# Performance work log

Hardware: AMD Instinct MI355X
Metric: run time of the kernel (lower is better)

Reference implementation:

```python
import jax, jax.numpy as jnp
import numpy as np

# Config (BERT-base with T5-style shared relative attention bias)
B, S, D, H, F, V, L = 16, 512, 768, 12, 3072, 30522, 12
DH = D // H
MAXREL = 128  # bias table has 2*MAXREL+1 = 257 buckets
EPS = 1e-12


def layer_norm(x, w, b):
    mu = jnp.mean(x, axis=-1, keepdims=True)
    var = jnp.mean(jnp.square(x - mu), axis=-1, keepdims=True)
    return (x - mu) * jax.lax.rsqrt(var + EPS) * w + b


def setup_inputs() -> dict:
    key = jax.random.key(0)
    ks = jax.random.split(key, 16)
    s = 0.02
    inp = {
        "input_ids": jax.random.randint(ks[0], (B, S), 0, V),
        "attention_mask": jnp.ones((B, S), jnp.float32),
        "word_emb": jax.random.normal(ks[1], (V, D), jnp.float32) * s,
        "pos_emb": jax.random.normal(ks[2], (S, D), jnp.float32) * s,
        "emb_ln_w": jnp.ones((D,), jnp.float32),
        "emb_ln_b": jnp.zeros((D,), jnp.float32),
        "rel_bias_table": jax.random.normal(ks[3], (2 * MAXREL + 1, H), jnp.float32) * s,
        "Wq": jax.random.normal(ks[4], (L, D, D), jnp.float32) * s,
        "bq": jnp.zeros((L, D), jnp.float32),
        "Wk": jax.random.normal(ks[5], (L, D, D), jnp.float32) * s,
        "bk": jnp.zeros((L, D), jnp.float32),
        "Wv": jax.random.normal(ks[6], (L, D, D), jnp.float32) * s,
        "bv": jnp.zeros((L, D), jnp.float32),
        "Wo": jax.random.normal(ks[7], (L, D, D), jnp.float32) * s,
        "bo": jnp.zeros((L, D), jnp.float32),
        "attn_ln_w": jnp.ones((L, D), jnp.float32),
        "attn_ln_b": jnp.zeros((L, D), jnp.float32),
        "Wi": jax.random.normal(ks[8], (L, F, D), jnp.float32) * s,
        "bi": jnp.zeros((L, F), jnp.float32),
        "Wd": jax.random.normal(ks[9], (L, D, F), jnp.float32) * s,
        "bd": jnp.zeros((L, D), jnp.float32),
        "out_ln_w": jnp.ones((L, D), jnp.float32),
        "out_ln_b": jnp.zeros((L, D), jnp.float32),
    }
    return inp


def _encoder(input_ids, attention_mask, word_emb, pos_emb, emb_ln_w, emb_ln_b,
             rel_bias_table, Wq, bq, Wk, bk, Wv, bv, Wo, bo, attn_ln_w, attn_ln_b,
             Wi, bi, Wd, bd, out_ln_w, out_ln_b):
    b, s = input_ids.shape
    # Embeddings: word + learned absolute position, then LayerNorm
    h = word_emb[input_ids] + pos_emb[:s][None, :, :]
    h = layer_norm(h, emb_ln_w, emb_ln_b)

    # Shared relative position bias: [H, S, S]
    pos = jnp.arange(s)
    rel = jnp.clip(pos[None, :] - pos[:, None], -MAXREL, MAXREL) + MAXREL
    rel_bias = jnp.transpose(rel_bias_table[rel], (2, 0, 1))[None]  # [1,H,S,S]

    # Additive attention mask: [B,1,1,S]
    add_mask = (1.0 - attention_mask)[:, None, None, :] * -10000.0
    scale = 1.0 / np.sqrt(DH)

    def step(h, p):
        wq, bq_, wk, bk_, wv, bv_, wo, bo_, lw1, lb1, wi, bi_, wd, bd_, lw2, lb2 = p
        q = (h @ wq.T + bq_).reshape(b, s, H, DH)
        k = (h @ wk.T + bk_).reshape(b, s, H, DH)
        v = (h @ wv.T + bv_).reshape(b, s, H, DH)
        scores = jnp.einsum('bqhd,bkhd->bhqk', q, k) * scale + rel_bias + add_mask
        attn = jax.nn.softmax(scores, axis=-1)
        ctx = jnp.einsum('bhqk,bkhd->bqhd', attn, v).reshape(b, s, D)
        h1 = layer_norm(h + (ctx @ wo.T + bo_), lw1, lb1)
        inter = jax.nn.gelu(h1 @ wi.T + bi_, approximate=False)
        h2 = layer_norm(h1 + (inter @ wd.T + bd_), lw2, lb2)
        return h2, None

    params = (Wq, bq, Wk, bk, Wv, bv, Wo, bo, attn_ln_w, attn_ln_b,
              Wi, bi, Wd, bd, out_ln_w, out_ln_b)
    h, _ = jax.lax.scan(step, h, params)
    return h


def reference(input_ids, attention_mask, word_emb, pos_emb, emb_ln_w, emb_ln_b,
              rel_bias_table, Wq, bq, Wk, bk, Wv, bv, Wo, bo, attn_ln_w, attn_ln_b,
              Wi, bi, Wd, bd, out_ln_w, out_ln_b):
    return _encoder(input_ids, attention_mask, word_emb, pos_emb, emb_ln_w, emb_ln_b,
                    rel_bias_table, Wq, bq, Wk, bk, Wv, bv, Wo, bo, attn_ln_w, attn_ln_b,
                    Wi, bi, Wd, bd, out_ln_w, out_ln_b)
```

## Files before the change

kernel.cpp:

```cpp
#include <hip/hip_runtime.h>
#include <cstdint>
#include <cstddef>

#define BB 16
#define SS 512
#define DD 768
#define HH 12
#define FF 3072
#define LL 12
#define DHD 64
#define MM (BB*SS)

typedef __attribute__((ext_vector_type(8))) short bf16x8;
typedef __attribute__((ext_vector_type(4))) float f32x4;

__device__ __forceinline__ ushort f2bf(float f) {
  union { float f; uint32_t u; } x; x.f = f;
  uint32_t r = x.u + 0x7FFFu + ((x.u >> 16) & 1u);
  return (ushort)(r >> 16);
}
__device__ __forceinline__ float bf2f(ushort u) {
  union { uint32_t u; float f; } x; x.u = (uint32_t)u << 16;
  return x.f;
}

__device__ __forceinline__ void glds16(const ushort* g, ushort* l) {
  __builtin_amdgcn_global_load_lds((__attribute__((address_space(1))) void*)g,
                                   (__attribute__((address_space(3))) void*)l,
                                   16, 0, 0);
}

__device__ __forceinline__ float gelu_t(float v) {
  const float v2 = v * v;
  const float u = v * (-1.5957691216f - 0.0713548163f * v2);
  return v / (1.f + __expf(u));
}

__global__ __launch_bounds__(256)
void convw6(const float* __restrict__ s0, const float* __restrict__ s1,
            const float* __restrict__ s2, const float* __restrict__ s3,
            const float* __restrict__ s4, const float* __restrict__ s5,
            ushort* __restrict__ dA, ushort* __restrict__ dB, int perD, int perF)
{
  const int y = blockIdx.y;
  const int per = (y < 4) ? perD : perF;
  const int i = (blockIdx.x * 256 + threadIdx.x) * 4;
  if (i >= per) return;
  const float* s = y == 0 ? s0 : y == 1 ? s1 : y == 2 ? s2 : y == 3 ? s3 : y == 4 ? s4 : s5;
  ushort* dst = (y < 4) ? (dA + (size_t)y * perD) : (dB + (size_t)(y - 4) * perF);
  const float4 v = *(const float4*)(s + i);
  ushort4 o;
  o.x = f2bf(v.x); o.y = f2bf(v.y); o.z = f2bf(v.z); o.w = f2bf(v.w);
  *(ushort4*)(dst + i) = o;
}

__global__ __launch_bounds__(256)
void embed_ln_kernel(const int* __restrict__ ids, const float* __restrict__ wemb,
                     const float* __restrict__ pemb, const float* __restrict__ g,
                     const float* __restrict__ bt, float* __restrict__ hf,
                     ushort* __restrict__ hb)
{
  const int row = blockIdx.x;
  const int s = row & (SS - 1);
  const int id = ids[row];
  const float* wp = wemb + (size_t)id * DD;
  const float* pp = pemb + (size_t)s * DD;
  const int tid = threadIdx.x;
  float v[3]; float sum = 0.f, sq = 0.f;
#pragma unroll
  for (int j = 0; j < 3; ++j) {
    int e = tid + j * 256;
    v[j] = wp[e] + pp[e];
    sum += v[j]; sq += v[j] * v[j];
  }
  __shared__ float red[2][4];
#pragma unroll
  for (int off = 32; off >= 1; off >>= 1) { sum += __shfl_xor(sum, off); sq += __shfl_xor(sq, off); }
  const int lane = tid & 63, wid = tid >> 6;
  if (lane == 0) { red[0][wid] = sum; red[1][wid] = sq; }
  __syncthreads();
  sum = red[0][0] + red[0][1] + red[0][2] + red[0][3];
  sq  = red[1][0] + red[1][1] + red[1][2] + red[1][3];
  const float mean = sum * (1.f / DD);
  const float var  = sq  * (1.f / DD) - mean * mean;
  const float rstd = rsqrtf(var + 1e-12f);
  const size_t base = (size_t)row * DD;
#pragma unroll
  for (int j = 0; j < 3; ++j) {
    int e = tid + j * 256;
    float o = (v[j] - mean) * rstd * g[e] + bt[e];
    hf[base + e] = o;
    hb[base + e] = f2bf(o);
  }
}

__global__ __launch_bounds__(256)
void add_ln2_kernel(const float* __restrict__ res, const ushort* __restrict__ p0,
                    const ushort* __restrict__ p1, const float* __restrict__ g,
                    const float* __restrict__ bt, float* __restrict__ hf,
                    ushort* __restrict__ hb)
{
  const int row = blockIdx.x;
  const int tid = threadIdx.x;
  const size_t base = (size_t)row * DD;
  float v[3]; float sum = 0.f, sq = 0.f;
#pragma unroll
  for (int j = 0; j < 3; ++j) {
    int e = tid + j * 256;
    v[j] = res[base + e] + bf2f(p0[base + e]) + bf2f(p1[base + e]);
    sum += v[j]; sq += v[j] * v[j];
  }
  __shared__ float red[2][4];
#pragma unroll
  for (int off = 32; off >= 1; off >>= 1) { sum += __shfl_xor(sum, off); sq += __shfl_xor(sq, off); }
  const int lane = tid & 63, wid = tid >> 6;
  if (lane == 0) { red[0][wid] = sum; red[1][wid] = sq; }
  __syncthreads();
  sum = red[0][0] + red[0][1] + red[0][2] + red[0][3];
  sq  = red[1][0] + red[1][1] + red[1][2] + red[1][3];
  const float mean = sum * (1.f / DD);
  const float var  = sq  * (1.f / DD) - mean * mean;
  const float rstd = rsqrtf(var + 1e-12f);
#pragma unroll
  for (int j = 0; j < 3; ++j) {
    int e = tid + j * 256;
    float o = (v[j] - mean) * rstd * g[e] + bt[e];
    hf[base + e] = o;
    hb[base + e] = f2bf(o);
  }
}

template<int EPI, bool TRV>
__global__ __launch_bounds__(256, 4)
void gemm_ker(const ushort* __restrict__ A,
              const ushort* __restrict__ B0, const ushort* __restrict__ B1,
              const ushort* __restrict__ B2,
              const float* __restrict__ bias0, const float* __restrict__ bias1,
              const float* __restrict__ bias2,
              void* __restrict__ C0, void* __restrict__ C1, void* __restrict__ C2,
              int Kdim, int nblk)
{
  __shared__ ushort As[2][128 * 32];
  __shared__ ushort Bs[2][128 * 32];

  int id = blockIdx.y * gridDim.x + blockIdx.x;
  const int chunk = (gridDim.x * gridDim.y) >> 3;
  id = (id & 7) * chunk + (id >> 3);
  const int bm = id & 63;
  const int bnAll = id >> 6;
  const int sub = bnAll / nblk;
  const int bn = bnAll - sub * nblk;

  const ushort* Bw  = sub == 0 ? B0 : (sub == 1 ? B1 : B2);
  const float* bias = sub == 0 ? bias0 : (sub == 1 ? bias1 : bias2);
  const int Ndim = nblk * 128;

  const int tid = threadIdx.x;
  const int l = tid & 63, w = tid >> 6;
  const int wm = w >> 1, wn = w & 1;
  const int fr = l & 15, fg = l >> 4;

  const int srow_in = l >> 2;
  const int gks = ((l & 3) ^ ((l >> 3) & 3)) * 8;
  const ushort* Agl0 = A  + (size_t)(bm * 128 + w * 16 + srow_in) * Kdim + gks;
  const ushort* Agl1 = Agl0 + (size_t)64 * Kdim;
  const ushort* Bgl0 = Bw + (size_t)(bn * 128 + w * 16 + srow_in) * Kdim + gks;
  const ushort* Bgl1 = Bgl0 + (size_t)64 * Kdim;

  auto stage = [&](int b, int kt) {
    const int ko = kt * 32;
    ushort* al = &As[b][w * 64 * 8];
    ushort* bl = &Bs[b][w * 64 * 8];
    glds16(Agl0 + ko, al);
    glds16(Agl1 + ko, al + 256 * 8);
    glds16(Bgl0 + ko, bl);
    glds16(Bgl1 + ko, bl + 256 * 8);
  };

  const int se = (fg ^ ((fr >> 1) & 3)) * 8;

  f32x4 acc[4][4];
#pragma unroll
  for (int i = 0; i < 4; ++i)
#pragma unroll
    for (int j = 0; j < 4; ++j) acc[i][j] = f32x4{0.f, 0.f, 0.f, 0.f};

  stage(0, 0);
  __syncthreads();

  const int nk = Kdim >> 5;
  int cur = 0;
  for (int kt = 0; kt < nk; ++kt) {
    if (kt + 1 < nk) stage(cur ^ 1, kt + 1);

    bf16x8 af[4], bfv[4];
#pragma unroll
    for (int i = 0; i < 4; ++i)
      af[i]  = *(const bf16x8*)&As[cur][(wm * 64 + i * 16 + fr) * 32 + se];
#pragma unroll
    for (int j = 0; j < 4; ++j)
      bfv[j] = *(const bf16x8*)&Bs[cur][(wn * 64 + j * 16 + fr) * 32 + se];

    __builtin_amdgcn_s_setprio(1);
#pragma unroll
    for (int i = 0; i < 4; ++i)
#pragma unroll
      for (int j = 0; j < 4; ++j)
        acc[i][j] = __builtin_amdgcn_mfma_f32_16x16x32_bf16(bfv[j], af[i], acc[i][j], 0, 0, 0);
    __builtin_amdgcn_s_setprio(0);

    __syncthreads();
    cur ^= 1;
  }

#pragma unroll
  for (int i = 0; i < 4; ++i) {
    const int row_g = bm * 128 + wm * 64 + i * 16 + fr;
#pragma unroll
    for (int j = 0; j < 4; ++j) {
      const int col = bn * 128 + wn * 64 + j * 16 + fg * 4;
      const float4 bv4 = *(const float4*)&bias[col];
      const float v0 = acc[i][j][0] + bv4.x;
      const float v1 = acc[i][j][1] + bv4.y;
      const float v2 = acc[i][j][2] + bv4.z;
      const float v3 = acc[i][j][3] + bv4.w;
      if (TRV && sub == 2) {
        const int b_ = row_g >> 9, s_ = row_g & 511;
        const int h_ = col >> 6, d0 = col & 63;
        ushort* vp = (ushort*)C2 + (((size_t)(b_ * HH + h_) * DHD + d0) * SS + s_);
        vp[0] = f2bf(v0); vp[SS] = f2bf(v1); vp[2 * SS] = f2bf(v2); vp[3 * SS] = f2bf(v3);
      } else if (EPI == 2) {
        ushort4 o4;
        o4.x = f2bf(gelu_t(v0)); o4.y = f2bf(gelu_t(v1));
        o4.z = f2bf(gelu_t(v2)); o4.w = f2bf(gelu_t(v3));
        *(ushort4*)&((ushort*)C0)[(size_t)row_g * Ndim + col] = o4;
      } else {
        void* Cout = sub == 0 ? C0 : (sub == 1 ? C1 : C2);
        ushort4 o4;
        o4.x = f2bf(v0); o4.y = f2bf(v1); o4.z = f2bf(v2); o4.w = f2bf(v3);
        *(ushort4*)&((ushort*)Cout)[(size_t)row_g * Ndim + col] = o4;
      }
    }
  }
}

__global__ __launch_bounds__(256, 4)
void gemm_sk(const ushort* __restrict__ A, const ushort* __restrict__ Bw,
             const float* __restrict__ bias, ushort* __restrict__ P0,
             ushort* __restrict__ P1, int Kdim)
{
  __shared__ ushort As[2][128 * 32];
  __shared__ ushort Bs[2][128 * 32];

  int id = blockIdx.y * gridDim.x + blockIdx.x;
  const int chunk = (gridDim.x * gridDim.y) >> 3;
  id = (id & 7) * chunk + (id >> 3);
  const int bm = id & 63;
  const int rest = id >> 6;
  const int bn = rest >> 1;
  const int sk = rest & 1;

  const int Kh = Kdim >> 1;

  const int tid = threadIdx.x;
  const int l = tid & 63, w = tid >> 6;
  const int wm = w >> 1, wn = w & 1;
  const int fr = l & 15, fg = l >> 4;

  const int srow_in = l >> 2;
  const int gks = ((l & 3) ^ ((l >> 3) & 3)) * 8;
  const ushort* Agl0 = A  + (size_t)(bm * 128 + w * 16 + srow_in) * Kdim + sk * Kh + gks;
  const ushort* Agl1 = Agl0 + (size_t)64 * Kdim;
  const ushort* Bgl0 = Bw + (size_t)(bn * 128 + w * 16 + srow_in) * Kdim + sk * Kh + gks;
  const ushort* Bgl1 = Bgl0 + (size_t)64 * Kdim;

  auto stage = [&](int b, int kt) {
    const int ko = kt * 32;
    ushort* al = &As[b][w * 64 * 8];
    ushort* bl = &Bs[b][w * 64 * 8];
    glds16(Agl0 + ko, al);
    glds16(Agl1 + ko, al + 256 * 8);
    glds16(Bgl0 + ko, bl);
    glds16(Bgl1 + ko, bl + 256 * 8);
  };

  const int se = (fg ^ ((fr >> 1) & 3)) * 8;

  f32x4 acc[4][4];
#pragma unroll
  for (int i = 0; i < 4; ++i)
#pragma unroll
    for (int j = 0; j < 4; ++j) acc[i][j] = f32x4{0.f, 0.f, 0.f, 0.f};

  stage(0, 0);
  __syncthreads();

  const int nk = Kh >> 5;
  int cur = 0;
  for (int kt = 0; kt < nk; ++kt) {
    if (kt + 1 < nk) stage(cur ^ 1, kt + 1);

    bf16x8 af[4], bfv[4];
#pragma unroll
    for (int i = 0; i < 4; ++i)
      af[i]  = *(const bf16x8*)&As[cur][(wm * 64 + i * 16 + fr) * 32 + se];
#pragma unroll
    for (int j = 0; j < 4; ++j)
      bfv[j] = *(const bf16x8*)&Bs[cur][(wn * 64 + j * 16 + fr) * 32 + se];

    __builtin_amdgcn_s_setprio(1);
#pragma unroll
    for (int i = 0; i < 4; ++i)
#pragma unroll
      for (int j = 0; j < 4; ++j)
        acc[i][j] = __builtin_amdgcn_mfma_f32_16x16x32_bf16(bfv[j], af[i], acc[i][j], 0, 0, 0);
    __builtin_amdgcn_s_setprio(0);

    __syncthreads();
    cur ^= 1;
  }

  ushort* P = sk ? P1 : P0;
  const float bs = sk ? 0.f : 1.f;
#pragma unroll
  for (int i = 0; i < 4; ++i) {
    const int row_g = bm * 128 + wm * 64 + i * 16 + fr;
#pragma unroll
    for (int j = 0; j < 4; ++j) {
      const int col = bn * 128 + wn * 64 + j * 16 + fg * 4;
      const float4 bv4 = *(const float4*)&bias[col];
      ushort4 o4;
      o4.x = f2bf(acc[i][j][0] + bv4.x * bs);
      o4.y = f2bf(acc[i][j][1] + bv4.y * bs);
      o4.z = f2bf(acc[i][j][2] + bv4.z * bs);
      o4.w = f2bf(acc[i][j][3] + bv4.w * bs);
      *(ushort4*)&P[(size_t)row_g * DD + col] = o4;
    }
  }
}

__global__ __launch_bounds__(512, 2)
void attn_kernel(const ushort* __restrict__ qb, const ushort* __restrict__ kb,
                 const ushort* __restrict__ vt, const float* __restrict__ relt,
                 const float* __restrict__ amask, ushort* __restrict__ ctxb)
{
  __shared__ ushort Kt[128][72];
  __shared__ ushort Vt[64][136];
  __shared__ ushort Pl[128][136];
  __shared__ float am_lds[512];
  __shared__ float rel_lds[1024];

  const int tid = threadIdx.x, lane = tid & 63, w = tid >> 6;

  int lin = blockIdx.y * gridDim.x + blockIdx.x;
  lin = (lin & 7) * 96 + (lin >> 3);
  const int qt = lin & 3;
  const int bh = lin >> 2;
  const int b = bh / HH, h = bh - b * HH;
  const int fr = lane & 15, fg = lane >> 4;

  am_lds[tid] = (1.0f - amask[b * SS + tid]) * -10000.0f;
  {
    int d0 = tid - 512;
    d0 = max(-128, d0);
    rel_lds[tid] = relt[(d0 + 128) * HH + h];
    int d1 = tid;
    d1 = min(128, d1);
    rel_lds[tid + 512] = relt[(d1 + 128) * HH + h];
  }

  bf16x8 qf[2];
  {
    const int qrow = qt * 128 + w * 16 + fr;
    const ushort* p = qb + ((size_t)(b * SS + qrow) * DD) + h * DHD + fg * 8;
    qf[0] = *(const bf16x8*)p;
    qf[1] = *(const bf16x8*)(p + 32);
  }

  f32x4 o[4];
  float mrow[4], lrow[4];
#pragma unroll
  for (int r = 0; r < 4; ++r) { mrow[r] = -1e30f; lrow[r] = 0.f; }
#pragma unroll
  for (int d = 0; d < 4; ++d) o[d] = f32x4{0.f, 0.f, 0.f, 0.f};

  const int skr = tid >> 2;
  const int shd = (tid & 3) * 16;
  const int vrow = tid >> 3;
  const int vcg  = (tid & 7) * 16;
  const ushort* vgl = vt + ((size_t)bh * DHD + vrow) * SS + vcg;

  const int qg0 = qt * 128 + w * 16;

  for (int kt = 0; kt < 4; ++kt) {
    const size_t gbase = ((size_t)(b * SS + kt * 128 + skr) * DD) + h * DHD + shd;
    int4 kr0 = *(const int4*)(kb + gbase);
    int4 kr1 = *(const int4*)(kb + gbase + 8);
    const ushort* vp = vgl + kt * 128;
    int4 vr0 = *(const int4*)(vp);
    int4 vr1 = *(const int4*)(vp + 8);

    __syncthreads();
    *(int4*)&Kt[skr][shd]     = kr0;
    *(int4*)&Kt[skr][shd + 8] = kr1;
    *(int4*)&Vt[vrow][vcg]     = vr0;
    *(int4*)&Vt[vrow][vcg + 8] = vr1;
    __syncthreads();

    float sv[8][4];
    __builtin_amdgcn_s_setprio(1);
#pragma unroll
    for (int kc = 0; kc < 8; ++kc) {
      f32x4 s = f32x4{0.f, 0.f, 0.f, 0.f};
      bf16x8 kf0 = *(const bf16x8*)&Kt[kc * 16 + fr][fg * 8];
      bf16x8 kf1 = *(const bf16x8*)&Kt[kc * 16 + fr][32 + fg * 8];
      s = __builtin_amdgcn_mfma_f32_16x16x32_bf16(qf[0], kf0, s, 0, 0, 0);
      s = __builtin_amdgcn_mfma_f32_16x16x32_bf16(qf[1], kf1, s, 0, 0, 0);
      const int col = kt * 128 + kc * 16 + fr;
      const float am = am_lds[col];
      const int ridx = col - qg0 - fg * 4 + 512;
#pragma unroll
      for (int r = 0; r < 4; ++r)
        sv[kc][r] = s[r] * 0.125f + rel_lds[ridx - r] + am;
    }
    __builtin_amdgcn_s_setprio(0);

    float ef[4];
#pragma unroll
    for (int r = 0; r < 4; ++r) {
      float tmax = sv[0][r];
#pragma unroll
      for (int kc = 1; kc < 8; ++kc) tmax = fmaxf(tmax, sv[kc][r]);
#pragma unroll
      for (int off = 1; off < 16; off <<= 1) tmax = fmaxf(tmax, __shfl_xor(tmax, off));
      const float mnew = fmaxf(mrow[r], tmax);
      ef[r] = __expf(mrow[r] - mnew);
      float psum = 0.f;
      const int prow = w * 16 + fg * 4 + r;
#pragma unroll
      for (int kc = 0; kc < 8; ++kc) {
        float p = __expf(sv[kc][r] - mnew);
        psum += p;
        Pl[prow][kc * 16 + fr] = f2bf(p);
      }
#pragma unroll
      for (int off = 1; off < 16; off <<= 1) psum += __shfl_xor(psum, off);
      lrow[r] = lrow[r] * ef[r] + psum;
      mrow[r] = mnew;
    }
#pragma unroll
    for (int dc = 0; dc < 4; ++dc)
#pragma unroll
      for (int r = 0; r < 4; ++r) o[dc][r] *= ef[r];
    __syncthreads();

    __builtin_amdgcn_s_setprio(1);
#pragma unroll
    for (int dc = 0; dc < 4; ++dc)
#pragma unroll
      for (int ks = 0; ks < 4; ++ks) {
        bf16x8 pf = *(const bf16x8*)&Pl[w * 16 + fr][ks * 32 + fg * 8];
        bf16x8 vf = *(const bf16x8*)&Vt[dc * 16 + fr][ks * 32 + fg * 8];
        o[dc] = __builtin_amdgcn_mfma_f32_16x16x32_bf16(pf, vf, o[dc], 0, 0, 0);
      }
    __builtin_amdgcn_s_setprio(0);
  }

#pragma unroll
  for (int dc = 0; dc < 4; ++dc)
#pragma unroll
    for (int r = 0; r < 4; ++r) {
      const int qg = qt * 128 + w * 16 + fg * 4 + r;
      const float v = o[dc][r] / lrow[r];
      ctxb[((size_t)(b * SS + qg) * DD) + h * DHD + dc * 16 + fr] = f2bf(v);
    }
}

extern "C" void kernel_launch(void* const* d_in, const int* in_sizes, int n_in,
                              void* d_out, int out_size, void* d_ws, size_t ws_size,
                              hipStream_t stream) {
  const int*   ids   = (const int*)d_in[0];
  const float* amask = (const float*)d_in[1];
  const float* wemb  = (const float*)d_in[2];
  const float* pemb  = (const float*)d_in[3];
  const float* eln_w = (const float*)d_in[4];
  const float* eln_b = (const float*)d_in[5];
  const float* relt  = (const float*)d_in[6];
  const float* Wq    = (const float*)d_in[7];
  const float* bq    = (const float*)d_in[8];
  const float* Wk    = (const float*)d_in[9];
  const float* bk    = (const float*)d_in[10];
  const float* Wv    = (const float*)d_in[11];
  const float* bv    = (const float*)d_in[12];
  const float* Wo    = (const float*)d_in[13];
  const float* bo    = (const float*)d_in[14];
  const float* aln_w = (const float*)d_in[15];
  const float* aln_b = (const float*)d_in[16];
  const float* Wi    = (const float*)d_in[17];
  const float* bi    = (const float*)d_in[18];
  const float* Wd    = (const float*)d_in[19];
  const float* bd    = (const float*)d_in[20];
  const float* oln_w = (const float*)d_in[21];
  const float* oln_b = (const float*)d_in[22];

  size_t off = 0;
  auto carve = [&](size_t bytes) -> void* {
    void* r = (char*)d_ws + off;
    off += (bytes + 255) & ~(size_t)255;
    return r;
  };
  float*  hf     = (float*) carve((size_t)MM * DD * 4);
  ushort* hb     = (ushort*)carve((size_t)MM * DD * 2);
  ushort* qbuf   = (ushort*)carve((size_t)MM * DD * 2);
  ushort* kbuf   = (ushort*)carve((size_t)MM * DD * 2);
  ushort* vbuf   = (ushort*)carve((size_t)MM * DD * 2);
  ushort* ctxb   = (ushort*)carve((size_t)MM * DD * 2);
  ushort* gout   = (ushort*)carve((size_t)MM * DD * 2);
  ushort* gout2  = (ushort*)carve((size_t)MM * DD * 2);
  ushort* interb = (ushort*)carve((size_t)MM * FF * 2);
  const int PD = DD * DD;
  const int PF = FF * DD;
  ushort* wBded  = (ushort*)carve((size_t)2 * PF * 2);

  ushort* wA = interb;

  embed_ln_kernel<<<MM, 256, 0, stream>>>(ids, wemb, pemb, eln_w, eln_b, hf, hb);

  const dim3 gQKV(MM / 128, 3 * (DD / 128));
  const dim3 gSK(MM / 128, 2 * (DD / 128));
  const dim3 gF(MM / 128, FF / 128);
  const dim3 gA(SS / 128, BB * HH);
  const dim3 gC(PF / 1024, 6);

  for (int l = 0; l < LL; ++l) {
    const size_t wo  = (size_t)l * PD;
    const size_t wio = (size_t)l * PF;

    convw6<<<gC, 256, 0, stream>>>(Wq + wo, Wk + wo, Wv + wo, Wo + wo,
                                   Wi + wio, Wd + wio, wA, wBded, PD, PF);

    gemm_ker<0, true><<<gQKV, 256, 0, stream>>>(hb, wA, wA + PD, wA + 2 * PD,
                                                bq + l * DD, bk + l * DD, bv + l * DD,
                                                qbuf, kbuf, vbuf, DD, DD / 128);

    attn_kernel<<<gA, 512, 0, stream>>>(qbuf, kbuf, vbuf, relt, amask, ctxb);

    gemm_sk<<<gSK, 256, 0, stream>>>(ctxb, wA + 3 * PD, bo + l * DD, gout, gout2, DD);
    add_ln2_kernel<<<MM, 256, 0, stream>>>(hf, gout, gout2,
                                           aln_w + l * DD, aln_b + l * DD, hf, hb);

    gemm_ker<2, false><<<gF, 256, 0, stream>>>(hb, wBded, wBded, wBded,
                                               bi + l * FF, bi + l * FF, bi + l * FF,
                                               interb, interb, interb, DD, FF / 128);
    gemm_sk<<<gSK, 256, 0, stream>>>(interb, wBded + PF, bd + l * DD, gout, gout2, FF);

    float* outp = (l == LL - 1) ? (float*)d_out : hf;
    add_ln2_kernel<<<MM, 256, 0, stream>>>(hf, gout, gout2,
                                           oln_w + l * DD, oln_b + l * DD, outp, hb);
  }
}
```

Baseline: 3.355 ms.

## Enlarge GEMM M-tile to 256 rows with 128x64 per-wave tiles

The main GEMM kernel's block tile grows from 128x128 to 256x128. Each wave now computes a 128x64 sub-tile with 32 accumulators instead of 16, and the QKV and FFN-up grids are halved along M. This raises the MFMA-to-LDS-load ratio and reuses each B tile across more rows, cutting shared-memory and global traffic per flop. The cost is more registers and LDS per block, so launch bounds drop to 2 blocks per CU, and fewer blocks may leave occupancy or tail balance worse.

```diff
diff --git a/kernel.cpp b/kernel.cpp
--- a/kernel.cpp
+++ b/kernel.cpp
@@ -131,7 +131,7 @@
 }
 
 template<int EPI, bool TRV>
-__global__ __launch_bounds__(256, 4)
+__global__ __launch_bounds__(256, 2)
 void gemm_ker(const ushort* __restrict__ A,
               const ushort* __restrict__ B0, const ushort* __restrict__ B1,
               const ushort* __restrict__ B2,
@@ -140,14 +140,14 @@
               void* __restrict__ C0, void* __restrict__ C1, void* __restrict__ C2,
               int Kdim, int nblk)
 {
-  __shared__ ushort As[2][128 * 32];
+  __shared__ ushort As[2][256 * 32];
   __shared__ ushort Bs[2][128 * 32];
 
   int id = blockIdx.y * gridDim.x + blockIdx.x;
   const int chunk = (gridDim.x * gridDim.y) >> 3;
   id = (id & 7) * chunk + (id >> 3);
-  const int bm = id & 63;
-  const int bnAll = id >> 6;
+  const int bm = id & 31;
+  const int bnAll = id >> 5;
   const int sub = bnAll / nblk;
   const int bn = bnAll - sub * nblk;
 
@@ -157,31 +157,32 @@
 
   const int tid = threadIdx.x;
   const int l = tid & 63, w = tid >> 6;
-  const int wm = w >> 1, wn = w & 1;
+  const int wr = w & 1, wc = w >> 1;
   const int fr = l & 15, fg = l >> 4;
 
   const int srow_in = l >> 2;
   const int gks = ((l & 3) ^ ((l >> 3) & 3)) * 8;
-  const ushort* Agl0 = A  + (size_t)(bm * 128 + w * 16 + srow_in) * Kdim + gks;
-  const ushort* Agl1 = Agl0 + (size_t)64 * Kdim;
-  const ushort* Bgl0 = Bw + (size_t)(bn * 128 + w * 16 + srow_in) * Kdim + gks;
-  const ushort* Bgl1 = Bgl0 + (size_t)64 * Kdim;
+  const ushort* Agl = A  + (size_t)(bm * 256 + w * 16 + srow_in) * Kdim + gks;
+  const ushort* Bgl = Bw + (size_t)(bn * 128 + w * 16 + srow_in) * Kdim + gks;
+  const size_t k64 = (size_t)64 * Kdim;
 
   auto stage = [&](int b, int kt) {
     const int ko = kt * 32;
-    ushort* al = &As[b][w * 64 * 8];
-    ushort* bl = &Bs[b][w * 64 * 8];
-    glds16(Agl0 + ko, al);
-    glds16(Agl1 + ko, al + 256 * 8);
-    glds16(Bgl0 + ko, bl);
-    glds16(Bgl1 + ko, bl + 256 * 8);
+    ushort* al = &As[b][w * 512];
+    ushort* bl = &Bs[b][w * 512];
+    glds16(Agl + ko,            al);
+    glds16(Agl + k64 + ko,      al + 2048);
+    glds16(Agl + 2 * k64 + ko,  al + 4096);
+    glds16(Agl + 3 * k64 + ko,  al + 6144);
+    glds16(Bgl + ko,            bl);
+    glds16(Bgl + k64 + ko,      bl + 2048);
   };
 
   const int se = (fg ^ ((fr >> 1) & 3)) * 8;
 
-  f32x4 acc[4][4];
-#pragma unroll
-  for (int i = 0; i < 4; ++i)
+  f32x4 acc[8][4];
+#pragma unroll
+  for (int i = 0; i < 8; ++i)
 #pragma unroll
     for (int j = 0; j < 4; ++j) acc[i][j] = f32x4{0.f, 0.f, 0.f, 0.f};
 
@@ -193,17 +194,17 @@
   for (int kt = 0; kt < nk; ++kt) {
     if (kt + 1 < nk) stage(cur ^ 1, kt + 1);
 
-    bf16x8 af[4], bfv[4];
-#pragma unroll
-    for (int i = 0; i < 4; ++i)
-      af[i]  = *(const bf16x8*)&As[cur][(wm * 64 + i * 16 + fr) * 32 + se];
+    bf16x8 af[8], bfv[4];
 #pragma unroll
     for (int j = 0; j < 4; ++j)
-      bfv[j] = *(const bf16x8*)&Bs[cur][(wn * 64 + j * 16 + fr) * 32 + se];
+      bfv[j] = *(const bf16x8*)&Bs[cur][(wc * 64 + j * 16 + fr) * 32 + se];
+#pragma unroll
+    for (int i = 0; i < 8; ++i)
+      af[i]  = *(const bf16x8*)&As[cur][(wr * 128 + i * 16 + fr) * 32 + se];
 
     __builtin_amdgcn_s_setprio(1);
 #pragma unroll
-    for (int i = 0; i < 4; ++i)
+    for (int i = 0; i < 8; ++i)
 #pragma unroll
       for (int j = 0; j < 4; ++j)
         acc[i][j] = __builtin_amdgcn_mfma_f32_16x16x32_bf16(bfv[j], af[i], acc[i][j], 0, 0, 0);
@@ -214,11 +215,11 @@
   }
 
 #pragma unroll
-  for (int i = 0; i < 4; ++i) {
-    const int row_g = bm * 128 + wm * 64 + i * 16 + fr;
+  for (int i = 0; i < 8; ++i) {
+    const int row_g = bm * 256 + wr * 128 + i * 16 + fr;
 #pragma unroll
     for (int j = 0; j < 4; ++j) {
-      const int col = bn * 128 + wn * 64 + j * 16 + fg * 4;
+      const int col = bn * 128 + wc * 64 + j * 16 + fg * 4;
       const float4 bv4 = *(const float4*)&bias[col];
       const float v0 = acc[i][j][0] + bv4.x;
       const float v1 = acc[i][j][1] + bv4.y;
@@ -526,9 +527,9 @@
 
   embed_ln_kernel<<<MM, 256, 0, stream>>>(ids, wemb, pemb, eln_w, eln_b, hf, hb);
 
-  const dim3 gQKV(MM / 128, 3 * (DD / 128));
+  const dim3 gQKV(MM / 256, 3 * (DD / 128));
   const dim3 gSK(MM / 128, 2 * (DD / 128));
-  const dim3 gF(MM / 128, FF / 128);
+  const dim3 gF(MM / 256, FF / 128);
   const dim3 gA(SS / 128, BB * HH);
   const dim3 gC(PF / 1024, 6);
 
```

Result: slower. 3.460 ms (+3.1%).
